# Kernel tuning notes

Hardware: AMD Instinct MI355X
Metric: run time of the kernel (lower is better)

## Reference

```python
import jax, jax.numpy as jnp
import numpy as np

H = 2048          # hidden_size
N = 16384         # batch (= events processed in one forward)
THR = 0.7         # event_threshold
NEG = -1e30       # masked-softmax fill


def setup_inputs() -> dict:
    key = jax.random.key(0)
    ks = jax.random.split(key, 8)
    s = lambda k, shape, scale: (jax.random.normal(k, shape, dtype=jnp.float32) * scale)
    return {
        "x": jax.random.normal(ks[0], (N, H), dtype=jnp.float32),
        "importance": jax.random.uniform(ks[1], (N,), dtype=jnp.float32),
        # event_detector: Linear(H, H//2) -> ReLU -> Linear(H//2, 1) -> Sigmoid
        "W_e1": s(ks[2], (H, H // 2), 0.02), "b_e1": jnp.zeros((H // 2,), jnp.float32),
        "W_e2": s(ks[3], (H // 2, 1), 0.05), "b_e2": jnp.ones((1,), jnp.float32),
        # retrieval_network: Linear(H, H//2) -> ReLU -> Linear(H//2, H) -> Sigmoid
        "W_r1": s(ks[4], (H, H // 2), 0.02), "b_r1": jnp.zeros((H // 2,), jnp.float32),
        "W_r2": s(ks[5], (H // 2, H), 0.02), "b_r2": jnp.zeros((H,), jnp.float32),
        "timestamp": 0,
    }


def reference(x, importance, W_e1, b_e1, W_e2, b_e2, W_r1, b_r1, W_r2, b_r2, timestamp):
    # --- detect_events: MLP -> sigmoid -> threshold -------------------------
    scores = jax.nn.sigmoid(jnp.maximum(x @ W_e1 + b_e1, 0.0) @ W_e2 + b_e2)[:, 0]  # [N]
    events = scores > THR                                   # bool mask = event-gated scatter
    has_events = jnp.any(events)

    # --- store_memory + consolidate_memories --------------------------------
    # Event rows are written into the ring buffer (no wraparound since N <= capacity);
    # consolidation = softmax over stored importances, weighted sum of stored rows.
    logits = jnp.where(events, importance, NEG)             # masked softmax over event rows
    w = jax.nn.softmax(logits)                              # [N]
    w = jnp.where(events, w, 0.0)
    consolidated = w @ x                                    # [H]

    # --- retrieve_memory -----------------------------------------------------
    # After consolidation memory_count == 1, so softmax(similarities) == 1 for
    # every query row and retrieved_memory == consolidated (broadcast to [N,H]).
    retrieved = jax.nn.sigmoid(jnp.maximum(consolidated @ W_r1 + b_r1, 0.0) @ W_r2 + b_r2)  # [H]

    # If no events fired, memory_count == 0 and retrieve_memory returns zeros.
    add = jnp.where(has_events, retrieved, jnp.zeros_like(retrieved))
    return x + add[None, :]
```

## Files before the change

kernel.cpp:

```cpp
#include <hip/hip_runtime.h>
#include <hip/hip_bf16.h>

#define H_    2048
#define NROWS 16384
#define HH    1024

typedef __bf16 bf16x8 __attribute__((ext_vector_type(8)));
typedef float  floatx4 __attribute__((ext_vector_type(4)));

__device__ __forceinline__ unsigned f2bf(float f) {
  unsigned u = __builtin_bit_cast(unsigned, f);
  u += 0x7fff + ((u >> 16) & 1);
  return u >> 16;
}

__device__ __forceinline__ void gload_lds16(const void* g, void* l) {
  __builtin_amdgcn_global_load_lds(
      (const __attribute__((address_space(1))) unsigned*)g,
      (__attribute__((address_space(3))) unsigned*)l, 16, 0, 0);
}

__global__ __launch_bounds__(256) void convert_x_kernel(
    const float* __restrict__ x, unsigned short* __restrict__ xb)
{
  size_t i = ((size_t)blockIdx.x * 256 + threadIdx.x) * 8;
  float4 v0 = *reinterpret_cast<const float4*>(x + i);
  float4 v1 = *reinterpret_cast<const float4*>(x + i + 4);
  uint4 o;
  o.x = f2bf(v0.x) | (f2bf(v0.y) << 16);
  o.y = f2bf(v0.z) | (f2bf(v0.w) << 16);
  o.z = f2bf(v1.x) | (f2bf(v1.y) << 16);
  o.w = f2bf(v1.z) | (f2bf(v1.w) << 16);
  *reinterpret_cast<uint4*>(xb + i) = o;
}

__global__ __launch_bounds__(256) void transpose_w1_kernel(
    const float* __restrict__ W1, unsigned short* __restrict__ W1t)
{
  __shared__ unsigned short tile[64][66];
  int k0 = blockIdx.x * 64;
  int n0 = blockIdx.y * 64;
  int t = threadIdx.x;
#pragma unroll
  for (int i = 0; i < 4; i++) {
    int idx = t + i * 256;
    int r = idx >> 4, c4 = (idx & 15) << 2;
    float4 v = *reinterpret_cast<const float4*>(W1 + (size_t)(k0 + r) * HH + n0 + c4);
    tile[r][c4 + 0] = (unsigned short)f2bf(v.x);
    tile[r][c4 + 1] = (unsigned short)f2bf(v.y);
    tile[r][c4 + 2] = (unsigned short)f2bf(v.z);
    tile[r][c4 + 3] = (unsigned short)f2bf(v.w);
  }
  __syncthreads();
#pragma unroll
  for (int i = 0; i < 2; i++) {
    int idx = t + i * 256;
    int n = idx >> 3, k8 = (idx & 7) << 3;
    uint4 o;
    o.x = (unsigned)tile[k8 + 0][n] | ((unsigned)tile[k8 + 1][n] << 16);
    o.y = (unsigned)tile[k8 + 2][n] | ((unsigned)tile[k8 + 3][n] << 16);
    o.z = (unsigned)tile[k8 + 4][n] | ((unsigned)tile[k8 + 5][n] << 16);
    o.w = (unsigned)tile[k8 + 6][n] | ((unsigned)tile[k8 + 7][n] << 16);
    *reinterpret_cast<uint4*>(W1t + (size_t)(n0 + n) * H_ + k0 + k8) = o;
  }
}

__global__ __launch_bounds__(256) void gemm_v2_kernel(
    const unsigned short* __restrict__ xb, const unsigned short* __restrict__ W1t,
    const float* __restrict__ b1, const float* __restrict__ W2,
    float* __restrict__ s_pre)
{
  __shared__ unsigned short As[128 * 64];
  __shared__ unsigned short Bs[128 * 64];

  const int t    = threadIdx.x;
  const int m0   = blockIdx.x * 128;
  const int n0   = blockIdx.y * 128;
  const int wave = t >> 6, lane = t & 63;
  const int wr   = (wave >> 1) * 64;
  const int wc   = (wave & 1) * 64;
  const int lcol = lane & 15, quad = lane >> 4;

  floatx4 acc[4][4] = {};

  const int srow = t >> 3;
  const int sq   = (t & 7) ^ (srow & 7);
  const unsigned short* ag = xb  + (size_t)(m0 + srow) * H_ + sq * 8;
  const unsigned short* bg = W1t + (size_t)(n0 + srow) * H_ + sq * 8;
  unsigned short* al = As + 512 * wave;
  unsigned short* bl = Bs + 512 * wave;

  for (int kk = 0; kk < H_; kk += 64) {
    __syncthreads();
#pragma unroll
    for (int j = 0; j < 4; j++) {
      gload_lds16(ag + kk + (size_t)(32 * j) * H_, al + 2048 * j);
      gload_lds16(bg + kk + (size_t)(32 * j) * H_, bl + 2048 * j);
    }
    __syncthreads();

#pragma unroll
    for (int h = 0; h < 2; h++) {
      bf16x8 af[4], bfr[4];
#pragma unroll
      for (int mt = 0; mt < 4; mt++) {
        int r = wr + mt * 16 + lcol;
        af[mt] = *reinterpret_cast<const bf16x8*>(
            As + r * 64 + ((((h << 2) | quad) ^ (r & 7)) << 3));
      }
#pragma unroll
      for (int nt = 0; nt < 4; nt++) {
        int r = wc + nt * 16 + lcol;
        bfr[nt] = *reinterpret_cast<const bf16x8*>(
            Bs + r * 64 + ((((h << 2) | quad) ^ (r & 7)) << 3));
      }
#pragma unroll
      for (int mt = 0; mt < 4; mt++)
#pragma unroll
        for (int nt = 0; nt < 4; nt++)
          acc[mt][nt] = __builtin_amdgcn_mfma_f32_16x16x32_bf16(af[mt], bfr[nt], acc[mt][nt], 0, 0, 0);
    }
  }

  float rowsum[4][4];
#pragma unroll
  for (int mt = 0; mt < 4; mt++)
#pragma unroll
    for (int r = 0; r < 4; r++) rowsum[mt][r] = 0.f;

#pragma unroll
  for (int nt = 0; nt < 4; nt++) {
    int n = n0 + wc + nt * 16 + lcol;
    float b1v = b1[n], w2v = W2[n];
#pragma unroll
    for (int mt = 0; mt < 4; mt++)
#pragma unroll
      for (int r = 0; r < 4; r++) {
        float h = fmaxf(acc[mt][nt][r] + b1v, 0.f);
        rowsum[mt][r] = fmaf(h, w2v, rowsum[mt][r]);
      }
  }
#pragma unroll
  for (int mt = 0; mt < 4; mt++)
#pragma unroll
    for (int r = 0; r < 4; r++) {
      float s = rowsum[mt][r];
      s += __shfl_xor(s, 1); s += __shfl_xor(s, 2);
      s += __shfl_xor(s, 4); s += __shfl_xor(s, 8);
      if (lcol == 0)
        atomicAdd(&s_pre[m0 + wr + mt * 16 + quad * 4 + r], s);
    }
}

__global__ __launch_bounds__(256) void gemm_score_kernel(
    const float* __restrict__ x, const float* __restrict__ W1,
    const float* __restrict__ b1, const float* __restrict__ W2,
    float* __restrict__ s_pre)
{
  __shared__ unsigned short As[128][40];
  __shared__ unsigned short Bs[128][40];
  const int t    = threadIdx.x;
  const int n0   = blockIdx.x * 128;
  const int m0   = blockIdx.y * 128;
  const int wave = t >> 6, lane = t & 63;
  const int wr   = (wave >> 1) * 64;
  const int wc   = (wave & 1) * 64;
  const int lcol = lane & 15, quad = lane >> 4;
  floatx4 acc[4][4] = {};

  for (int kk = 0; kk < H_; kk += 32) {
    __syncthreads();
#pragma unroll
    for (int i = 0; i < 4; i++) {
      int idx = t + i * 256;
      int row = idx >> 3, k4 = (idx & 7) << 2;
      float4 v = *reinterpret_cast<const float4*>(x + (size_t)(m0 + row) * H_ + kk + k4);
      unsigned lo = f2bf(v.x) | (f2bf(v.y) << 16);
      unsigned hi = f2bf(v.z) | (f2bf(v.w) << 16);
      *reinterpret_cast<uint2*>(&As[row][k4]) = make_uint2(lo, hi);
    }
#pragma unroll
    for (int i = 0; i < 4; i++) {
      int idx = t + i * 256;
      int kr = idx >> 5, c4 = (idx & 31) << 2;
      float4 v = *reinterpret_cast<const float4*>(W1 + (size_t)(kk + kr) * HH + n0 + c4);
      Bs[c4 + 0][kr] = (unsigned short)f2bf(v.x);
      Bs[c4 + 1][kr] = (unsigned short)f2bf(v.y);
      Bs[c4 + 2][kr] = (unsigned short)f2bf(v.z);
      Bs[c4 + 3][kr] = (unsigned short)f2bf(v.w);
    }
    __syncthreads();
    bf16x8 af[4], bfr[4];
#pragma unroll
    for (int mt = 0; mt < 4; mt++)
      af[mt] = *reinterpret_cast<const bf16x8*>(&As[wr + mt * 16 + lcol][quad * 8]);
#pragma unroll
    for (int nt = 0; nt < 4; nt++)
      bfr[nt] = *reinterpret_cast<const bf16x8*>(&Bs[wc + nt * 16 + lcol][quad * 8]);
#pragma unroll
    for (int mt = 0; mt < 4; mt++)
#pragma unroll
      for (int nt = 0; nt < 4; nt++)
        acc[mt][nt] = __builtin_amdgcn_mfma_f32_16x16x32_bf16(af[mt], bfr[nt], acc[mt][nt], 0, 0, 0);
  }
  float rowsum[4][4];
#pragma unroll
  for (int mt = 0; mt < 4; mt++)
#pragma unroll
    for (int r = 0; r < 4; r++) rowsum[mt][r] = 0.f;
#pragma unroll
  for (int nt = 0; nt < 4; nt++) {
    int n = n0 + wc + nt * 16 + lcol;
    float b1v = b1[n], w2v = W2[n];
#pragma unroll
    for (int mt = 0; mt < 4; mt++)
#pragma unroll
      for (int r = 0; r < 4; r++) {
        float h = fmaxf(acc[mt][nt][r] + b1v, 0.f);
        rowsum[mt][r] = fmaf(h, w2v, rowsum[mt][r]);
      }
  }
#pragma unroll
  for (int mt = 0; mt < 4; mt++)
#pragma unroll
    for (int r = 0; r < 4; r++) {
      float s = rowsum[mt][r];
      s += __shfl_xor(s, 1); s += __shfl_xor(s, 2);
      s += __shfl_xor(s, 4); s += __shfl_xor(s, 8);
      if (lcol == 0)
        atomicAdd(&s_pre[m0 + wr + mt * 16 + quad * 4 + r], s);
    }
}

__global__ __launch_bounds__(256) void score_kernel(
    const float* __restrict__ s_pre, const float* __restrict__ imp,
    const float* __restrict__ b2, float* __restrict__ wbuf,
    float* __restrict__ Z, float* __restrict__ cnt)
{
  int i = blockIdx.x * 256 + threadIdx.x;
  float s = s_pre[i] + b2[0];
  float sig = 1.f / (1.f + __expf(-s));
  bool ev = sig > 0.7f;
  float w = ev ? __expf(imp[i]) : 0.f;
  wbuf[i] = w;
  float cw = ev ? 1.f : 0.f;
#pragma unroll
  for (int off = 32; off; off >>= 1) {
    w  += __shfl_down(w, off);
    cw += __shfl_down(cw, off);
  }
  if ((threadIdx.x & 63) == 0) {
    atomicAdd(Z, w);
    atomicAdd(cnt, cw);
  }
}

__global__ __launch_bounds__(256) void consolidate_kernel(
    const float* __restrict__ x, const float* __restrict__ wbuf,
    float* __restrict__ c)
{
  int t = threadIdx.x;
  int r0 = blockIdx.x * 32;
  float a[8] = {0.f, 0.f, 0.f, 0.f, 0.f, 0.f, 0.f, 0.f};
  for (int r = 0; r < 32; r++) {
    float w = wbuf[r0 + r];
    if (w != 0.f) {
      const float4* xr = reinterpret_cast<const float4*>(x + (size_t)(r0 + r) * H_);
      float4 v0 = xr[t], v1 = xr[t + 256];
      a[0] = fmaf(w, v0.x, a[0]); a[1] = fmaf(w, v0.y, a[1]);
      a[2] = fmaf(w, v0.z, a[2]); a[3] = fmaf(w, v0.w, a[3]);
      a[4] = fmaf(w, v1.x, a[4]); a[5] = fmaf(w, v1.y, a[5]);
      a[6] = fmaf(w, v1.z, a[6]); a[7] = fmaf(w, v1.w, a[7]);
    }
  }
  int j0 = t * 4;
  atomicAdd(&c[j0 + 0], a[0]); atomicAdd(&c[j0 + 1], a[1]);
  atomicAdd(&c[j0 + 2], a[2]); atomicAdd(&c[j0 + 3], a[3]);
  atomicAdd(&c[1024 + j0 + 0], a[4]); atomicAdd(&c[1024 + j0 + 1], a[5]);
  atomicAdd(&c[1024 + j0 + 2], a[6]); atomicAdd(&c[1024 + j0 + 3], a[7]);
}

__global__ __launch_bounds__(256) void r1_kernel(
    const float* __restrict__ c, const float* __restrict__ Z,
    const float* __restrict__ cnt, const float* __restrict__ Wr1,
    float* __restrict__ hr)
{
  __shared__ float cs[128];
  int n  = blockIdx.x * 256 + threadIdx.x;
  int k0 = blockIdx.y * 128;
  float inv = (cnt[0] > 0.5f) ? (1.f / Z[0]) : 0.f;
  if (threadIdx.x < 128) cs[threadIdx.x] = c[k0 + threadIdx.x] * inv;
  __syncthreads();
  float s = 0.f;
#pragma unroll 8
  for (int k = 0; k < 128; k++)
    s = fmaf(cs[k], Wr1[(size_t)(k0 + k) * HH + n], s);
  atomicAdd(&hr[n], s);
}

__global__ __launch_bounds__(256) void r2_kernel(
    const float* __restrict__ hr, const float* __restrict__ br1,
    const float* __restrict__ Wr2, float* __restrict__ rt)
{
  __shared__ float hs[128];
  int n  = blockIdx.x * 256 + threadIdx.x;
  int k0 = blockIdx.y * 128;
  if (threadIdx.x < 128)
    hs[threadIdx.x] = fmaxf(hr[k0 + threadIdx.x] + br1[k0 + threadIdx.x], 0.f);
  __syncthreads();
  float s = 0.f;
#pragma unroll 8
  for (int k = 0; k < 128; k++)
    s = fmaf(hs[k], Wr2[(size_t)(k0 + k) * H_ + n], s);
  atomicAdd(&rt[n], s);
}

__global__ __launch_bounds__(256) void finalize_kernel(
    const float* __restrict__ rt, const float* __restrict__ br2,
    const float* __restrict__ cnt, float* __restrict__ addv)
{
  int j = blockIdx.x * 256 + threadIdx.x;
  float v = 0.f;
  if (cnt[0] > 0.5f) v = 1.f / (1.f + expf(-(rt[j] + br2[j])));
  addv[j] = v;
}

__global__ __launch_bounds__(256) void out_kernel(
    const float* __restrict__ x, const float* __restrict__ addv,
    float* __restrict__ out)
{
  size_t i = (size_t)blockIdx.x * 256 + threadIdx.x;
  int j4 = (int)(i & 511);
  float4 a = reinterpret_cast<const float4*>(addv)[j4];
  float4 v = reinterpret_cast<const float4*>(x)[i];
  v.x += a.x; v.y += a.y; v.z += a.z; v.w += a.w;
  reinterpret_cast<float4*>(out)[i] = v;
}

extern "C" void kernel_launch(void* const* d_in, const int* in_sizes, int n_in,
                              void* d_out, int out_size, void* d_ws, size_t ws_size,
                              hipStream_t stream)
{
  (void)in_sizes; (void)n_in; (void)out_size;
  const float* x   = (const float*)d_in[0];
  const float* imp = (const float*)d_in[1];
  const float* We1 = (const float*)d_in[2];
  const float* be1 = (const float*)d_in[3];
  const float* We2 = (const float*)d_in[4];
  const float* be2 = (const float*)d_in[5];
  const float* Wr1 = (const float*)d_in[6];
  const float* br1 = (const float*)d_in[7];
  const float* Wr2 = (const float*)d_in[8];
  const float* br2 = (const float*)d_in[9];
  float* out = (float*)d_out;

  float* ws    = (float*)d_ws;
  float* s_pre = ws;
  float* c     = ws + 16384;
  float* hr    = ws + 18432;
  float* rt    = ws + 19456;
  float* Z     = ws + 21504;
  float* cnt   = ws + 21505;
  float* wbuf  = ws + 21760;
  float* addv  = ws + 38144;

  const size_t scal_bytes = 49152 * sizeof(float);
  const size_t xb_bytes   = (size_t)NROWS * H_ * 2;
  const size_t w1t_bytes  = (size_t)HH * H_ * 2;
  unsigned short* xb  = (unsigned short*)((char*)d_ws + scal_bytes);
  unsigned short* W1t = (unsigned short*)((char*)d_ws + scal_bytes + xb_bytes);
  const bool fast = ws_size >= scal_bytes + xb_bytes + w1t_bytes;

  hipMemsetAsync(d_ws, 0, 21506 * sizeof(float), stream);

  if (fast) {
    convert_x_kernel<<<16384, 256, 0, stream>>>(x, xb);
    transpose_w1_kernel<<<dim3(32, 16), 256, 0, stream>>>(We1, W1t);
    gemm_v2_kernel<<<dim3(128, 8), 256, 0, stream>>>(xb, W1t, be1, We2, s_pre);
  } else {
    gemm_score_kernel<<<dim3(8, 128), 256, 0, stream>>>(x, We1, be1, We2, s_pre);
  }
  score_kernel<<<64, 256, 0, stream>>>(s_pre, imp, be2, wbuf, Z, cnt);
  consolidate_kernel<<<512, 256, 0, stream>>>(x, wbuf, c);
  r1_kernel<<<dim3(4, 16), 256, 0, stream>>>(c, Z, cnt, Wr1, hr);
  r2_kernel<<<dim3(8, 8), 256, 0, stream>>>(hr, br1, Wr2, rt);
  finalize_kernel<<<8, 256, 0, stream>>>(rt, br2, cnt, addv);
  out_kernel<<<32768, 256, 0, stream>>>(x, addv, out);
}
```

Before: 456.1 us.

## Fuse scoring into consolidation with deterministic partial sums; grid-stride elementwise kernels

```diff
diff --git a/kernel.cpp b/kernel.cpp
--- a/kernel.cpp
+++ b/kernel.cpp
@@ -23,15 +23,19 @@
 __global__ __launch_bounds__(256) void convert_x_kernel(
     const float* __restrict__ x, unsigned short* __restrict__ xb)
 {
-  size_t i = ((size_t)blockIdx.x * 256 + threadIdx.x) * 8;
-  float4 v0 = *reinterpret_cast<const float4*>(x + i);
-  float4 v1 = *reinterpret_cast<const float4*>(x + i + 4);
-  uint4 o;
-  o.x = f2bf(v0.x) | (f2bf(v0.y) << 16);
-  o.y = f2bf(v0.z) | (f2bf(v0.w) << 16);
-  o.z = f2bf(v1.x) | (f2bf(v1.y) << 16);
-  o.w = f2bf(v1.z) | (f2bf(v1.w) << 16);
-  *reinterpret_cast<uint4*>(xb + i) = o;
+  size_t base = ((size_t)blockIdx.x * 256 + threadIdx.x) * 8;
+#pragma unroll
+  for (int it = 0; it < 8; ++it) {
+    size_t i = base + (size_t)it * (524288u * 8);
+    float4 v0 = *reinterpret_cast<const float4*>(x + i);
+    float4 v1 = *reinterpret_cast<const float4*>(x + i + 4);
+    uint4 o;
+    o.x = f2bf(v0.x) | (f2bf(v0.y) << 16);
+    o.y = f2bf(v0.z) | (f2bf(v0.w) << 16);
+    o.z = f2bf(v1.x) | (f2bf(v1.y) << 16);
+    o.w = f2bf(v1.z) | (f2bf(v1.w) << 16);
+    *reinterpret_cast<uint4*>(xb + i) = o;
+  }
 }
 
 __global__ __launch_bounds__(256) void transpose_w1_kernel(
@@ -232,6 +236,61 @@
     }
 }
 
+__global__ __launch_bounds__(256) void consolidate_partial_kernel(
+    const float* __restrict__ x, const float* __restrict__ s_pre,
+    const float* __restrict__ imp, const float* __restrict__ b2,
+    float* __restrict__ part, float* __restrict__ Z, float* __restrict__ cnt)
+{
+  __shared__ float wl[64];
+  int t  = threadIdx.x;
+  int r0 = blockIdx.x * 64;
+  if (t < 64) {
+    float s   = s_pre[r0 + t] + b2[0];
+    float sig = 1.f / (1.f + __expf(-s));
+    bool  ev  = sig > 0.7f;
+    float w   = ev ? __expf(imp[r0 + t]) : 0.f;
+    wl[t] = w;
+    float cw = ev ? 1.f : 0.f;
+#pragma unroll
+    for (int off = 32; off; off >>= 1) {
+      w  += __shfl_down(w, off);
+      cw += __shfl_down(cw, off);
+    }
+    if (t == 0) { atomicAdd(Z, w); atomicAdd(cnt, cw); }
+  }
+  __syncthreads();
+
+  float a[8] = {0.f, 0.f, 0.f, 0.f, 0.f, 0.f, 0.f, 0.f};
+  for (int r = 0; r < 64; ++r) {
+    float w = wl[r];
+    if (w != 0.f) {
+      const float4* xr = reinterpret_cast<const float4*>(x + (size_t)(r0 + r) * H_);
+      float4 v0 = xr[t], v1 = xr[t + 256];
+      a[0] = fmaf(w, v0.x, a[0]); a[1] = fmaf(w, v0.y, a[1]);
+      a[2] = fmaf(w, v0.z, a[2]); a[3] = fmaf(w, v0.w, a[3]);
+      a[4] = fmaf(w, v1.x, a[4]); a[5] = fmaf(w, v1.y, a[5]);
+      a[6] = fmaf(w, v1.z, a[6]); a[7] = fmaf(w, v1.w, a[7]);
+    }
+  }
+  size_t base = (size_t)blockIdx.x * 2048;
+  int j0 = t * 4;
+  part[base + j0 + 0] = a[0]; part[base + j0 + 1] = a[1];
+  part[base + j0 + 2] = a[2]; part[base + j0 + 3] = a[3];
+  part[base + 1024 + j0 + 0] = a[4]; part[base + 1024 + j0 + 1] = a[5];
+  part[base + 1024 + j0 + 2] = a[6]; part[base + 1024 + j0 + 3] = a[7];
+}
+
+__global__ __launch_bounds__(256) void reduce_c_kernel(
+    const float* __restrict__ part, float* __restrict__ c)
+{
+  int j = blockIdx.x * 256 + threadIdx.x;
+  float s = 0.f;
+#pragma unroll 8
+  for (int b = 0; b < 256; ++b)
+    s += part[(size_t)b * 2048 + j];
+  c[j] = s;
+}
+
 __global__ __launch_bounds__(256) void score_kernel(
     const float* __restrict__ s_pre, const float* __restrict__ imp,
     const float* __restrict__ b2, float* __restrict__ wbuf,
@@ -260,9 +319,9 @@
     float* __restrict__ c)
 {
   int t = threadIdx.x;
-  int r0 = blockIdx.x * 32;
+  int r0 = blockIdx.x * 128;
   float a[8] = {0.f, 0.f, 0.f, 0.f, 0.f, 0.f, 0.f, 0.f};
-  for (int r = 0; r < 32; r++) {
+  for (int r = 0; r < 128; r++) {
     float w = wbuf[r0 + r];
     if (w != 0.f) {
       const float4* xr = reinterpret_cast<const float4*>(x + (size_t)(r0 + r) * H_);
@@ -329,12 +388,15 @@
     const float* __restrict__ x, const float* __restrict__ addv,
     float* __restrict__ out)
 {
-  size_t i = (size_t)blockIdx.x * 256 + threadIdx.x;
-  int j4 = (int)(i & 511);
-  float4 a = reinterpret_cast<const float4*>(addv)[j4];
-  float4 v = reinterpret_cast<const float4*>(x)[i];
-  v.x += a.x; v.y += a.y; v.z += a.z; v.w += a.w;
-  reinterpret_cast<float4*>(out)[i] = v;
+  size_t base = (size_t)blockIdx.x * 256 + threadIdx.x;
+  float4 a = reinterpret_cast<const float4*>(addv)[(int)(base & 511)];
+#pragma unroll
+  for (int it = 0; it < 16; ++it) {
+    size_t i = base + (size_t)it * 524288u;
+    float4 v = reinterpret_cast<const float4*>(x)[i];
+    v.x += a.x; v.y += a.y; v.z += a.z; v.w += a.w;
+    reinterpret_cast<float4*>(out)[i] = v;
+  }
 }
 
 extern "C" void kernel_launch(void* const* d_in, const int* in_sizes, int n_in,
@@ -369,21 +431,24 @@
   const size_t w1t_bytes  = (size_t)HH * H_ * 2;
   unsigned short* xb  = (unsigned short*)((char*)d_ws + scal_bytes);
   unsigned short* W1t = (unsigned short*)((char*)d_ws + scal_bytes + xb_bytes);
+  float* part = (float*)xb;
   const bool fast = ws_size >= scal_bytes + xb_bytes + w1t_bytes;
 
   hipMemsetAsync(d_ws, 0, 21506 * sizeof(float), stream);
 
   if (fast) {
-    convert_x_kernel<<<16384, 256, 0, stream>>>(x, xb);
+    convert_x_kernel<<<2048, 256, 0, stream>>>(x, xb);
     transpose_w1_kernel<<<dim3(32, 16), 256, 0, stream>>>(We1, W1t);
     gemm_v2_kernel<<<dim3(128, 8), 256, 0, stream>>>(xb, W1t, be1, We2, s_pre);
+    consolidate_partial_kernel<<<256, 256, 0, stream>>>(x, s_pre, imp, be2, part, Z, cnt);
+    reduce_c_kernel<<<8, 256, 0, stream>>>(part, c);
   } else {
     gemm_score_kernel<<<dim3(8, 128), 256, 0, stream>>>(x, We1, be1, We2, s_pre);
-  }
-  score_kernel<<<64, 256, 0, stream>>>(s_pre, imp, be2, wbuf, Z, cnt);
-  consolidate_kernel<<<512, 256, 0, stream>>>(x, wbuf, c);
+    score_kernel<<<64, 256, 0, stream>>>(s_pre, imp, be2, wbuf, Z, cnt);
+    consolidate_kernel<<<128, 256, 0, stream>>>(x, wbuf, c);
+  }
   r1_kernel<<<dim3(4, 16), 256, 0, stream>>>(c, Z, cnt, Wr1, hr);
   r2_kernel<<<dim3(8, 8), 256, 0, stream>>>(hr, br1, Wr2, rt);
   finalize_kernel<<<8, 256, 0, stream>>>(rt, br2, cnt, addv);
-  out_kernel<<<32768, 256, 0, stream>>>(x, addv, out);
-}
+  out_kernel<<<2048, 256, 0, stream>>>(x, addv, out);
+}
```

Measured after the change: 443.4 us. 2.8% less time.
